# Optimization experiments

Hardware: AMD Instinct MI355X
Metric: run time of the kernel (lower is better)

Reference implementation:

```python
import jax, jax.numpy as jnp
import numpy as np

N_EMBD = 768
NUM_EXPERTS = 64
EXPERT_WIDTH = 256            # all experts uniform width (expert_sizes=[(64,256)])
TOTAL_WIDTH = NUM_EXPERTS * EXPERT_WIDTH  # 16384
TOP_K = 8


def setup_inputs() -> dict:
    key = jax.random.key(0)
    k1, k2, k3, k4 = jax.random.split(key, 4)
    B, S = 1, 2048
    x = jax.random.normal(k1, (B, S, N_EMBD), dtype=jnp.float32)
    # router: nn.Linear(n_embd, num_experts, bias=False) -> weight [E, n_embd]
    router_w = jax.random.normal(k2, (NUM_EXPERTS, N_EMBD), dtype=jnp.float32) * 0.02
    # trunc_normal(std=0.02) approximated by clipped normal
    w1 = jnp.clip(jax.random.normal(k3, (N_EMBD, TOTAL_WIDTH), dtype=jnp.float32) * 0.02, -0.06, 0.06)
    w2 = jnp.clip(jax.random.normal(k4, (TOTAL_WIDTH, N_EMBD), dtype=jnp.float32) * 0.02, -0.06, 0.06)
    return {"x": x, "router_w": router_w, "w1": w1, "w2": w2}


def reference(x, router_w, w1, w2):
    B, S, D = x.shape
    T = B * S
    x_flat = x.reshape(T, D)

    # Router: sigmoid gating + top-k
    router_logits = x_flat @ router_w.T                      # [T, E]
    router_probs = jax.nn.sigmoid(router_logits.astype(jnp.float32))
    top_k_weights, selected_experts = jax.lax.top_k(router_probs, TOP_K)  # [T, K]
    top_k_weights = top_k_weights / (top_k_weights.sum(axis=-1, keepdims=True) + 1e-20)
    top_k_weights = top_k_weights.astype(x.dtype)

    # Per-token expert combine weights [T, E]: 0 for unselected experts.
    tok_idx = jnp.arange(T)[:, None]
    w_tok = jnp.zeros((T, NUM_EXPERTS), dtype=x.dtype).at[tok_idx, selected_experts].set(top_k_weights)

    # Expert MLP (relu^2 activation), dense-masked equivalent of
    # padded_gather -> grouped GEMM -> padded_scatter.
    h = jnp.square(jax.nn.relu(x_flat @ w1))                 # [T, E*W]
    h = (h.reshape(T, NUM_EXPERTS, EXPERT_WIDTH) * w_tok[:, :, None]).reshape(T, TOTAL_WIDTH)
    output = (h @ w2).reshape(B, S, D)

    # Aux losses
    router_z_loss = jnp.mean(jnp.square(jax.nn.logsumexp(router_logits, axis=-1)))
    tokens_per_expert = jnp.zeros((NUM_EXPERTS,), dtype=jnp.float32).at[selected_experts.reshape(-1)].add(1.0)
    f_i = (tokens_per_expert / tokens_per_expert.sum()).astype(x.dtype)
    p_i = router_probs.mean(axis=0)
    # all expert widths equal -> num_experts * (f_i . p_i)
    load_balance_loss = NUM_EXPERTS * (f_i.astype(jnp.float32) @ p_i)
    # expert_widths_normalized == ones -> mean over tokens of sum of probs
    compute_loss = router_probs.sum(axis=-1).mean()

    return output, router_z_loss, load_balance_loss, compute_loss, f_i
```

## Files before the change

### kernel.cpp

```cpp
#include <hip/hip_runtime.h>
#include <hip/hip_bf16.h>

#define T_TOKENS 2048
#define D_EMBD 768
#define N_EXP 64
#define EW 256
#define TOPK 8
#define TW (N_EXP*EW)
#define PAD_SLOTS 20480
#define SCHED_MAX 2560
#define OUT_BASE (2048*768)

typedef __attribute__((ext_vector_type(8))) short bf16x8;
typedef __attribute__((ext_vector_type(4))) float f32x4;

typedef __attribute__((address_space(1))) void GAS;
typedef __attribute__((address_space(3))) void LAS;
#define GLOAD16(g, l) __builtin_amdgcn_global_load_lds((GAS*)(g), (LAS*)(l), 16, 0, 0)

__global__ void k_init(int* counts, int* cursor, float* psum, float* scal,
                       float* wgt_slot, int* tok_slot, int* sched_e) {
  int i = blockIdx.x*256 + threadIdx.x;
  if (i < N_EXP) { counts[i] = 0; cursor[i] = 0; psum[i] = 0.f; }
  if (i < 2) scal[i] = 0.f;
  if (i < PAD_SLOTS) { wgt_slot[i] = 0.f; tok_slot[i] = 0; }
  if (i < SCHED_MAX) sched_e[i] = -1;
}

__global__ void k_cvt_x(const float* __restrict__ x, __hip_bfloat16* __restrict__ xb) {
  int i = blockIdx.x*256 + threadIdx.x;
  float4 v = reinterpret_cast<const float4*>(x)[i];
  union { __hip_bfloat16 b; unsigned short u; } c0, c1, c2, c3;
  c0.b = __float2bfloat16(v.x); c1.b = __float2bfloat16(v.y);
  c2.b = __float2bfloat16(v.z); c3.b = __float2bfloat16(v.w);
  ushort4 o; o.x = c0.u; o.y = c1.u; o.z = c2.u; o.w = c3.u;
  reinterpret_cast<ushort4*>(xb)[i] = o;
}

__global__ __launch_bounds__(256) void k_transpose_cvt(
    const float* __restrict__ s1, __hip_bfloat16* __restrict__ d1,
    const float* __restrict__ s2, __hip_bfloat16* __restrict__ d2) {
  __shared__ float t[64][65];
  const float* src; __hip_bfloat16* dst; int R, C, bx, by;
  if (blockIdx.z == 0) { src = s1; dst = d1; R = 768; C = 16384;
                         bx = blockIdx.x*64; by = blockIdx.y*64; }
  else                 { src = s2; dst = d2; R = 16384; C = 768;
                         bx = blockIdx.y*64; by = blockIdx.x*64; }
  int tid = threadIdx.x;
  int lr = tid >> 4, lc4 = tid & 15;
  #pragma unroll
  for (int i = 0; i < 4; i++) {
    int r = lr + i*16;
    float4 v = *reinterpret_cast<const float4*>(&src[(size_t)(by+r)*C + bx + lc4*4]);
    t[r][lc4*4+0] = v.x; t[r][lc4*4+1] = v.y; t[r][lc4*4+2] = v.z; t[r][lc4*4+3] = v.w;
  }
  __syncthreads();
  int a = tid & 7, b0 = tid >> 3;
  int r0 = a*8;
  #pragma unroll
  for (int pass = 0; pass < 2; pass++) {
    int c = b0 + pass*32;
    unsigned int w[8];
    #pragma unroll
    for (int j = 0; j < 8; j++) {
      union { __hip_bfloat16 b; unsigned short u; } cv;
      cv.b = __float2bfloat16(t[r0+j][c]);
      w[j] = cv.u;
    }
    uint4 o;
    o.x = w[0] | (w[1] << 16);
    o.y = w[2] | (w[3] << 16);
    o.z = w[4] | (w[5] << 16);
    o.w = w[6] | (w[7] << 16);
    *reinterpret_cast<uint4*>(&dst[(size_t)(bx+c)*R + by + r0]) = o;
  }
}

__global__ __launch_bounds__(256) void k_logits(const float* __restrict__ x,
                                                const float* __restrict__ rw,
                                                float* __restrict__ lp) {
  __shared__ float rw_s[8][256];
  int tid = threadIdx.x;
  int tg = blockIdx.x, eg = blockIdx.y, kc = blockIdx.z;
  #pragma unroll
  for (int idx = 0; idx < 8; idx++)
    rw_s[idx][tid] = rw[(size_t)(eg*8 + idx)*D_EMBD + kc*256 + tid];
  __syncthreads();
  int tok = tg*256 + tid;
  const float4* x4 = reinterpret_cast<const float4*>(x + (size_t)tok*D_EMBD + kc*256);
  float acc[8];
  #pragma unroll
  for (int e = 0; e < 8; e++) acc[e] = 0.f;
  #pragma unroll 4
  for (int k4 = 0; k4 < 64; k4++) {
    float4 xv = x4[k4];
    #pragma unroll
    for (int e = 0; e < 8; e++)
      acc[e] += xv.x*rw_s[e][k4*4+0] + xv.y*rw_s[e][k4*4+1]
              + xv.z*rw_s[e][k4*4+2] + xv.w*rw_s[e][k4*4+3];
  }
  float* dst = lp + (size_t)kc*T_TOKENS*N_EXP + (size_t)tok*N_EXP + eg*8;
  float4 o0 = {acc[0], acc[1], acc[2], acc[3]};
  float4 o1 = {acc[4], acc[5], acc[6], acc[7]};
  reinterpret_cast<float4*>(dst)[0] = o0;
  reinterpret_cast<float4*>(dst)[1] = o1;
}

__global__ __launch_bounds__(256) void k_router2(const float* __restrict__ lp,
                          int* __restrict__ sel_e, float* __restrict__ sel_w,
                          int* __restrict__ counts, float* __restrict__ psum,
                          float* __restrict__ scal) {
  __shared__ float psum_s[4][64];
  __shared__ int cnt_s[4][64];
  int tid = threadIdx.x, wv = tid >> 6, lane = tid & 63;
  float pacc = 0.f, zacc = 0.f;
  int cacc = 0;
  int tbase = blockIdx.x*8 + wv*2;
  #pragma unroll
  for (int it = 0; it < 2; it++) {
    int t = tbase + it;
    float logit = lp[(size_t)t*N_EXP + lane]
                + lp[(size_t)T_TOKENS*N_EXP + (size_t)t*N_EXP + lane]
                + lp[2*(size_t)T_TOKENS*N_EXP + (size_t)t*N_EXP + lane];
    float prob = 1.f/(1.f + expf(-logit));
    pacc += prob;
    float mx = logit;
    for (int s = 32; s; s >>= 1) mx = fmaxf(mx, __shfl_xor(mx, s, 64));
    float sse = expf(logit - mx);
    for (int s = 32; s; s >>= 1) sse += __shfl_xor(sse, s, 64);
    float lse = mx + logf(sse);
    zacc += lse*lse;
    int rank = 0;
    #pragma unroll
    for (int j = 0; j < 64; j++) {
      float pj = __shfl(prob, j, 64);
      rank += (pj > prob || (pj == prob && j < lane)) ? 1 : 0;
    }
    bool sel = rank < TOPK;
    float sp = sel ? prob : 0.f;
    for (int s = 32; s; s >>= 1) sp += __shfl_xor(sp, s, 64);
    if (sel) {
      sel_e[t*TOPK + rank] = lane;
      sel_w[t*TOPK + rank] = prob / (sp + 1e-20f);
      cacc++;
    }
  }
  psum_s[wv][lane] = pacc;
  cnt_s[wv][lane] = cacc;
  if (lane == 0) atomicAdd(&scal[0], zacc);
  __syncthreads();
  if (tid < 64) {
    float p = psum_s[0][tid] + psum_s[1][tid] + psum_s[2][tid] + psum_s[3][tid];
    int c = cnt_s[0][tid] + cnt_s[1][tid] + cnt_s[2][tid] + cnt_s[3][tid];
    atomicAdd(&psum[tid], p);
    atomicAdd(&counts[tid], c);
  }
}

__global__ void k_schedule(const int* __restrict__ counts, int* __restrict__ offsets,
                           int* __restrict__ sched_e, int* __restrict__ sched_r0) {
  int e = threadIdx.x;
  int c = counts[e];
  int tiles = (c + 63) >> 6;
  int padded = tiles << 6;
  int ip = padded;
  for (int s = 1; s < 64; s <<= 1) { int v = __shfl_up(ip, s, 64); if (e >= s) ip += v; }
  int rowoff = ip - padded;
  offsets[e] = rowoff;
  int it = tiles;
  for (int s = 8; s < 64; s <<= 1) { int v = __shfl_up(it, s, 64); if (e >= s) it += v; }
  int rank = it - tiles;
  int xcd = e & 7;
  for (int i = 0; i < tiles; i++) {
    int p = xcd + 8*(rank + i);
    sched_e[p] = e;
    sched_r0[p] = rowoff + i*64;
  }
}

__global__ void k_assign(const int* __restrict__ sel_e, const float* __restrict__ sel_w,
                         const int* __restrict__ offsets, int* __restrict__ cursor,
                         int* __restrict__ tok_slot, float* __restrict__ wgt_slot,
                         int* __restrict__ slot_tk) {
  int i = blockIdx.x*256 + threadIdx.x;
  int e = sel_e[i];
  int pos = atomicAdd(&cursor[e], 1);
  int slot = offsets[e] + pos;
  tok_slot[slot] = i >> 3;
  wgt_slot[slot] = sel_w[i];
  slot_tk[i] = slot;
}

template<int MODE>
__global__ __launch_bounds__(256) void k_moe_gemm(
    const __hip_bfloat16* __restrict__ Ab, const __hip_bfloat16* __restrict__ Bt,
    const int* __restrict__ sched_e, const int* __restrict__ sched_r0,
    const int* __restrict__ tok_slot, const float* __restrict__ wgt_slot,
    __hip_bfloat16* __restrict__ outp) {
  constexpr int NS = (MODE == 1) ? 12 : 4;
  __shared__ __hip_bfloat16 As[2][64*64];
  __shared__ __hip_bfloat16 Bs[2][128*64];
  int tid = threadIdx.x;
  int nch = blockIdx.y;
  int arl = tid >> 3, akc = tid & 7;
  int a_off = ((akc ^ (arl & 7)) << 3);
  int b_off = a_off;
  int wv = tid >> 6, lane = tid & 63;
  int wm = wv >> 1, wn = wv & 1;
  int l15 = lane & 15, l4 = lane >> 4;
  int b_str = (MODE == 1) ? D_EMBD : TW;

  for (int p = blockIdx.x; p < SCHED_MAX; p += gridDim.x) {
    int e = sched_e[p];
    if (e < 0) continue;
    int r0 = sched_r0[p];

    size_t a_base0, a_base1;
    if (MODE == 1) {
      a_base0 = (size_t)tok_slot[r0 + arl] * D_EMBD;
      a_base1 = (size_t)tok_slot[r0 + arl + 32] * D_EMBD;
    } else {
      a_base0 = (size_t)(r0 + arl) * EW;
      a_base1 = (size_t)(r0 + arl + 32) * EW;
    }
    size_t b_base = (MODE == 1) ? (size_t)(e*EW + nch*128) * D_EMBD
                                : (size_t)(nch*128) * TW + (size_t)e*EW;

    f32x4 acc[2][4];
    f32x4 z = {0.f, 0.f, 0.f, 0.f};
    #pragma unroll
    for (int m = 0; m < 2; m++)
      #pragma unroll
      for (int n = 0; n < 4; n++) acc[m][n] = z;

    auto STAGE = [&](int bsel, int k0) {
      GLOAD16(Ab + a_base0 + k0 + a_off, &As[bsel][0] + tid*8);
      GLOAD16(Ab + a_base1 + k0 + a_off, &As[bsel][0] + (256 + tid)*8);
      #pragma unroll
      for (int i = 0; i < 4; i++) {
        int br = i*32 + arl;
        GLOAD16(Bt + b_base + (size_t)br*b_str + k0 + b_off, &Bs[bsel][0] + (i*256 + tid)*8);
      }
    };

    int cur = 0;
    STAGE(0, 0);
    asm volatile("s_waitcnt vmcnt(0)" ::: "memory");
    __syncthreads();
    for (int step = 0; step < NS; step++) {
      if (step + 1 < NS) STAGE(cur ^ 1, (step + 1)*64);
      const bf16x8* A8 = reinterpret_cast<const bf16x8*>(&As[cur][0]);
      const bf16x8* B8 = reinterpret_cast<const bf16x8*>(&Bs[cur][0]);
      bf16x8 af[2][2], bq[4][2];
      #pragma unroll
      for (int m = 0; m < 2; m++) {
        int ra = wm*32 + m*16 + l15;
        #pragma unroll
        for (int kk = 0; kk < 2; kk++)
          af[m][kk] = A8[ra*8 + ((kk*4 + l4) ^ (ra & 7))];
      }
      #pragma unroll
      for (int n = 0; n < 4; n++) {
        int rb = wn*64 + n*16 + l15;
        #pragma unroll
        for (int kk = 0; kk < 2; kk++)
          bq[n][kk] = B8[rb*8 + ((kk*4 + l4) ^ (rb & 7))];
      }
      #pragma unroll
      for (int kk = 0; kk < 2; kk++)
        #pragma unroll
        for (int m = 0; m < 2; m++)
          #pragma unroll
          for (int n = 0; n < 4; n++)
            acc[m][n] = __builtin_amdgcn_mfma_f32_16x16x32_bf16(af[m][kk], bq[n][kk], acc[m][n], 0, 0, 0);
      asm volatile("s_waitcnt vmcnt(0)" ::: "memory");
      __syncthreads();
      cur ^= 1;
    }

    if (MODE == 1) {
      #pragma unroll
      for (int m = 0; m < 2; m++)
        #pragma unroll
        for (int j = 0; j < 4; j++) {
          int r = r0 + wm*32 + m*16 + l4*4 + j;
          float wg = wgt_slot[r];
          #pragma unroll
          for (int n = 0; n < 4; n++) {
            int col = nch*128 + wn*64 + n*16 + l15;
            float v = fmaxf(acc[m][n][j], 0.f);
            outp[(size_t)r*EW + col] = __float2bfloat16(v*v*wg);
          }
        }
    } else {
      #pragma unroll
      for (int m = 0; m < 2; m++)
        #pragma unroll
        for (int j = 0; j < 4; j++) {
          int r = r0 + wm*32 + m*16 + l4*4 + j;
          #pragma unroll
          for (int n = 0; n < 4; n++) {
            int col = nch*128 + wn*64 + n*16 + l15;
            outp[(size_t)r*D_EMBD + col] = __float2bfloat16(acc[m][n][j]);
          }
        }
    }
  }
}

__global__ void k_combine(const __hip_bfloat16* __restrict__ y, const int* __restrict__ slot_tk,
                          float* __restrict__ out) {
  __shared__ int s[TOPK];
  int t = blockIdx.x, tid = threadIdx.x;
  if (tid < TOPK) s[tid] = slot_tk[t*TOPK + tid];
  __syncthreads();
  if (tid < 192) {
    int c = tid*4;
    float a0 = 0.f, a1 = 0.f, a2 = 0.f, a3 = 0.f;
    #pragma unroll
    for (int k = 0; k < TOPK; k++) {
      ushort4 v = *reinterpret_cast<const ushort4*>(&y[(size_t)s[k]*D_EMBD + c]);
      union { unsigned int u; float f; } f0, f1, f2, f3;
      f0.u = ((unsigned int)v.x) << 16;
      f1.u = ((unsigned int)v.y) << 16;
      f2.u = ((unsigned int)v.z) << 16;
      f3.u = ((unsigned int)v.w) << 16;
      a0 += f0.f; a1 += f1.f; a2 += f2.f; a3 += f3.f;
    }
    float4 o = {a0, a1, a2, a3};
    *reinterpret_cast<float4*>(&out[(size_t)t*D_EMBD + c]) = o;
  }
}

__global__ void k_finalize(const int* __restrict__ counts, const float* __restrict__ psum,
                           const float* __restrict__ scal, float* __restrict__ out) {
  __shared__ float part[N_EXP], ptot[N_EXP];
  int e = threadIdx.x;
  float f = (float)counts[e] / 16384.f;
  float p = psum[e] / 2048.f;
  part[e] = f * p;
  ptot[e] = p;
  out[OUT_BASE + 3 + e] = f;
  __syncthreads();
  if (e == 0) {
    float s = 0.f, q = 0.f;
    for (int i = 0; i < N_EXP; i++) { s += part[i]; q += ptot[i]; }
    out[OUT_BASE + 0] = scal[0] / 2048.f;
    out[OUT_BASE + 1] = 64.f * s;
    out[OUT_BASE + 2] = q;
  }
}

extern "C" void kernel_launch(void* const* d_in, const int* in_sizes, int n_in,
                              void* d_out, int out_size, void* d_ws, size_t ws_size,
                              hipStream_t stream) {
  const float* x  = (const float*)d_in[0];
  const float* rw = (const float*)d_in[1];
  const float* w1 = (const float*)d_in[2];
  const float* w2 = (const float*)d_in[3];
  float* out = (float*)d_out;
  char* ws = (char*)d_ws;

  size_t o = 0;
  auto alloc = [&](size_t b) { size_t r = o; o += (b + 255) & ~(size_t)255; return r; };
  __hip_bfloat16* xb    = (__hip_bfloat16*)(ws + alloc(2048UL*768*2));
  __hip_bfloat16* w1t   = (__hip_bfloat16*)(ws + alloc(16384UL*768*2));
  __hip_bfloat16* w2t   = (__hip_bfloat16*)(ws + alloc(768UL*16384*2));
  __hip_bfloat16* hprm  = (__hip_bfloat16*)(ws + alloc((size_t)PAD_SLOTS*256*2));
  __hip_bfloat16* yprm  = (__hip_bfloat16*)(ws + alloc((size_t)PAD_SLOTS*768*2));
  float* lp      = (float*)(ws + alloc(3UL*2048*64*4));
  int*   sel_e   = (int*)  (ws + alloc(16384UL*4));
  float* sel_w   = (float*)(ws + alloc(16384UL*4));
  int*   slot_tk = (int*)  (ws + alloc(16384UL*4));
  int*   tokslot = (int*)  (ws + alloc((size_t)PAD_SLOTS*4));
  float* wgtslot = (float*)(ws + alloc((size_t)PAD_SLOTS*4));
  int*   counts  = (int*)  (ws + alloc(256));
  int*   cursor  = (int*)  (ws + alloc(256));
  float* psum    = (float*)(ws + alloc(256));
  float* scal    = (float*)(ws + alloc(256));
  int*   offsets = (int*)  (ws + alloc(256));
  int*   sch_e   = (int*)  (ws + alloc(SCHED_MAX*4));
  int*   sch_r0  = (int*)  (ws + alloc(SCHED_MAX*4));

  k_init<<<80, 256, 0, stream>>>(counts, cursor, psum, scal, wgtslot, tokslot, sch_e);
  k_cvt_x<<<1536, 256, 0, stream>>>(x, xb);
  k_transpose_cvt<<<dim3(256, 12, 2), 256, 0, stream>>>(w1, w1t, w2, w2t);
  k_logits<<<dim3(8, 8, 3), 256, 0, stream>>>(x, rw, lp);
  k_router2<<<256, 256, 0, stream>>>(lp, sel_e, sel_w, counts, psum, scal);
  k_schedule<<<1, 64, 0, stream>>>(counts, offsets, sch_e, sch_r0);
  k_assign<<<64, 256, 0, stream>>>(sel_e, sel_w, offsets, cursor, tokslot, wgtslot, slot_tk);
  k_moe_gemm<1><<<dim3(512, 2), 256, 0, stream>>>(xb, w1t, sch_e, sch_r0, tokslot, wgtslot, hprm);
  k_moe_gemm<2><<<dim3(512, 6), 256, 0, stream>>>(hprm, w2t, sch_e, sch_r0, tokslot, wgtslot, yprm);
  k_combine<<<2048, 256, 0, stream>>>(yprm, slot_tk, out);
  k_finalize<<<1, 64, 0, stream>>>(counts, psum, scal, out);
}
```

Baseline: 143.4 us.

## Shrink MoE row tiles to 32, keep GEMM2 A-tile resident, batch transpose tiles

Expert row padding drops from 64 to 32 rows, which cuts wasted padded rows in both grouped GEMMs. The schedule array grows to match. GEMM2 now loads the full 32x256 A tile into LDS once and loops over three 128-column output chunks per block, instead of reloading A for each of six y-blocks. The weight transpose kernel handles four 64x64 tiles per block and prefetches the next tile's loads into registers while converting the current one. Smaller M tiles halve the MFMA work per B-tile load, so weight traffic per useful FLOP goes up.

Result: slower. 164.8 us (+14.9%).

```diff
diff --git a/kernel.cpp b/kernel.cpp
--- a/kernel.cpp
+++ b/kernel.cpp
@@ -8,7 +8,7 @@
 #define TOPK 8
 #define TW (N_EXP*EW)
 #define PAD_SLOTS 20480
-#define SCHED_MAX 2560
+#define SCHED_MAX 4608
 #define OUT_BASE (2048*768)
 
 typedef __attribute__((ext_vector_type(8))) short bf16x8;
@@ -41,38 +41,57 @@
     const float* __restrict__ s1, __hip_bfloat16* __restrict__ d1,
     const float* __restrict__ s2, __hip_bfloat16* __restrict__ d2) {
   __shared__ float t[64][65];
-  const float* src; __hip_bfloat16* dst; int R, C, bx, by;
+  const float* src; __hip_bfloat16* dst; int R, C;
+  int ro_base, co_base, ro_step, co_step;
   if (blockIdx.z == 0) { src = s1; dst = d1; R = 768; C = 16384;
-                         bx = blockIdx.x*64; by = blockIdx.y*64; }
+                         ro_base = blockIdx.y*64; co_base = blockIdx.x*256;
+                         ro_step = 0; co_step = 64; }
   else                 { src = s2; dst = d2; R = 16384; C = 768;
-                         bx = blockIdx.y*64; by = blockIdx.x*64; }
+                         ro_base = blockIdx.x*256; co_base = blockIdx.y*64;
+                         ro_step = 64; co_step = 0; }
   int tid = threadIdx.x;
   int lr = tid >> 4, lc4 = tid & 15;
+  int a = tid & 7, b0 = tid >> 3;
+
+  float4 v[4];
   #pragma unroll
-  for (int i = 0; i < 4; i++) {
-    int r = lr + i*16;
-    float4 v = *reinterpret_cast<const float4*>(&src[(size_t)(by+r)*C + bx + lc4*4]);
-    t[r][lc4*4+0] = v.x; t[r][lc4*4+1] = v.y; t[r][lc4*4+2] = v.z; t[r][lc4*4+3] = v.w;
-  }
-  __syncthreads();
-  int a = tid & 7, b0 = tid >> 3;
-  int r0 = a*8;
-  #pragma unroll
-  for (int pass = 0; pass < 2; pass++) {
-    int c = b0 + pass*32;
-    unsigned int w[8];
-    #pragma unroll
-    for (int j = 0; j < 8; j++) {
-      union { __hip_bfloat16 b; unsigned short u; } cv;
-      cv.b = __float2bfloat16(t[r0+j][c]);
-      w[j] = cv.u;
-    }
-    uint4 o;
-    o.x = w[0] | (w[1] << 16);
-    o.y = w[2] | (w[3] << 16);
-    o.z = w[4] | (w[5] << 16);
-    o.w = w[6] | (w[7] << 16);
-    *reinterpret_cast<uint4*>(&dst[(size_t)(bx+c)*R + by + r0]) = o;
+  for (int i = 0; i < 4; i++)
+    v[i] = *reinterpret_cast<const float4*>(&src[(size_t)(ro_base + lr + i*16)*C + co_base + lc4*4]);
+
+  for (int q = 0; q < 4; q++) {
+    int ro = ro_base + q*ro_step, co = co_base + q*co_step;
+    __syncthreads();
+    #pragma unroll
+    for (int i = 0; i < 4; i++) {
+      int r = lr + i*16;
+      t[r][lc4*4+0] = v[i].x; t[r][lc4*4+1] = v[i].y;
+      t[r][lc4*4+2] = v[i].z; t[r][lc4*4+3] = v[i].w;
+    }
+    __syncthreads();
+    if (q < 3) {
+      int ro2 = ro_base + (q+1)*ro_step, co2 = co_base + (q+1)*co_step;
+      #pragma unroll
+      for (int i = 0; i < 4; i++)
+        v[i] = *reinterpret_cast<const float4*>(&src[(size_t)(ro2 + lr + i*16)*C + co2 + lc4*4]);
+    }
+    int r0 = a*8;
+    #pragma unroll
+    for (int pass = 0; pass < 2; pass++) {
+      int c = b0 + pass*32;
+      unsigned int w[8];
+      #pragma unroll
+      for (int j = 0; j < 8; j++) {
+        union { __hip_bfloat16 b; unsigned short u; } cv;
+        cv.b = __float2bfloat16(t[r0+j][c]);
+        w[j] = cv.u;
+      }
+      uint4 o;
+      o.x = w[0] | (w[1] << 16);
+      o.y = w[2] | (w[3] << 16);
+      o.z = w[4] | (w[5] << 16);
+      o.w = w[6] | (w[7] << 16);
+      *reinterpret_cast<uint4*>(&dst[(size_t)(co + c)*R + ro + r0]) = o;
+    }
   }
 }
 
@@ -161,8 +180,8 @@
                            int* __restrict__ sched_e, int* __restrict__ sched_r0) {
   int e = threadIdx.x;
   int c = counts[e];
-  int tiles = (c + 63) >> 6;
-  int padded = tiles << 6;
+  int tiles = (c + 31) >> 5;
+  int padded = tiles << 5;
   int ip = padded;
   for (int s = 1; s < 64; s <<= 1) { int v = __shfl_up(ip, s, 64); if (e >= s) ip += v; }
   int rowoff = ip - padded;
@@ -174,7 +193,7 @@
   for (int i = 0; i < tiles; i++) {
     int p = xcd + 8*(rank + i);
     sched_e[p] = e;
-    sched_r0[p] = rowoff + i*64;
+    sched_r0[p] = rowoff + i*32;
   }
 }
 
@@ -191,55 +210,40 @@
   slot_tk[i] = slot;
 }
 
-template<int MODE>
-__global__ __launch_bounds__(256) void k_moe_gemm(
+__global__ __launch_bounds__(256) void k_gemm1(
     const __hip_bfloat16* __restrict__ Ab, const __hip_bfloat16* __restrict__ Bt,
     const int* __restrict__ sched_e, const int* __restrict__ sched_r0,
     const int* __restrict__ tok_slot, const float* __restrict__ wgt_slot,
     __hip_bfloat16* __restrict__ outp) {
-  constexpr int NS = (MODE == 1) ? 12 : 4;
-  __shared__ __hip_bfloat16 As[2][64*64];
+  __shared__ __hip_bfloat16 As[2][32*64];
   __shared__ __hip_bfloat16 Bs[2][128*64];
   int tid = threadIdx.x;
   int nch = blockIdx.y;
   int arl = tid >> 3, akc = tid & 7;
   int a_off = ((akc ^ (arl & 7)) << 3);
-  int b_off = a_off;
   int wv = tid >> 6, lane = tid & 63;
   int wm = wv >> 1, wn = wv & 1;
   int l15 = lane & 15, l4 = lane >> 4;
-  int b_str = (MODE == 1) ? D_EMBD : TW;
 
   for (int p = blockIdx.x; p < SCHED_MAX; p += gridDim.x) {
     int e = sched_e[p];
     if (e < 0) continue;
     int r0 = sched_r0[p];
 
-    size_t a_base0, a_base1;
-    if (MODE == 1) {
-      a_base0 = (size_t)tok_slot[r0 + arl] * D_EMBD;
-      a_base1 = (size_t)tok_slot[r0 + arl + 32] * D_EMBD;
-    } else {
-      a_base0 = (size_t)(r0 + arl) * EW;
-      a_base1 = (size_t)(r0 + arl + 32) * EW;
-    }
-    size_t b_base = (MODE == 1) ? (size_t)(e*EW + nch*128) * D_EMBD
-                                : (size_t)(nch*128) * TW + (size_t)e*EW;
-
-    f32x4 acc[2][4];
+    size_t a_base = (size_t)tok_slot[r0 + arl] * D_EMBD;
+    size_t b_base = (size_t)(e*EW + nch*128) * D_EMBD;
+
+    f32x4 acc[4];
     f32x4 z = {0.f, 0.f, 0.f, 0.f};
     #pragma unroll
-    for (int m = 0; m < 2; m++)
-      #pragma unroll
-      for (int n = 0; n < 4; n++) acc[m][n] = z;
+    for (int n = 0; n < 4; n++) acc[n] = z;
 
     auto STAGE = [&](int bsel, int k0) {
-      GLOAD16(Ab + a_base0 + k0 + a_off, &As[bsel][0] + tid*8);
-      GLOAD16(Ab + a_base1 + k0 + a_off, &As[bsel][0] + (256 + tid)*8);
+      GLOAD16(Ab + a_base + k0 + a_off, &As[bsel][0] + tid*8);
       #pragma unroll
       for (int i = 0; i < 4; i++) {
         int br = i*32 + arl;
-        GLOAD16(Bt + b_base + (size_t)br*b_str + k0 + b_off, &Bs[bsel][0] + (i*256 + tid)*8);
+        GLOAD16(Bt + b_base + (size_t)br*D_EMBD + k0 + a_off, &Bs[bsel][0] + (i*256 + tid)*8);
       }
     };
 
@@ -247,18 +251,15 @@
     STAGE(0, 0);
     asm volatile("s_waitcnt vmcnt(0)" ::: "memory");
     __syncthreads();
-    for (int step = 0; step < NS; step++) {
-      if (step + 1 < NS) STAGE(cur ^ 1, (step + 1)*64);
+    for (int step = 0; step < 12; step++) {
+      if (step + 1 < 12) STAGE(cur ^ 1, (step + 1)*64);
       const bf16x8* A8 = reinterpret_cast<const bf16x8*>(&As[cur][0]);
       const bf16x8* B8 = reinterpret_cast<const bf16x8*>(&Bs[cur][0]);
-      bf16x8 af[2][2], bq[4][2];
-      #pragma unroll
-      for (int m = 0; m < 2; m++) {
-        int ra = wm*32 + m*16 + l15;
-        #pragma unroll
-        for (int kk = 0; kk < 2; kk++)
-          af[m][kk] = A8[ra*8 + ((kk*4 + l4) ^ (ra & 7))];
-      }
+      bf16x8 af[2], bq[4][2];
+      int ra = wm*16 + l15;
+      #pragma unroll
+      for (int kk = 0; kk < 2; kk++)
+        af[kk] = A8[ra*8 + ((kk*4 + l4) ^ (ra & 7))];
       #pragma unroll
       for (int n = 0; n < 4; n++) {
         int rb = wn*64 + n*16 + l15;
@@ -269,41 +270,112 @@
       #pragma unroll
       for (int kk = 0; kk < 2; kk++)
         #pragma unroll
-        for (int m = 0; m < 2; m++)
-          #pragma unroll
-          for (int n = 0; n < 4; n++)
-            acc[m][n] = __builtin_amdgcn_mfma_f32_16x16x32_bf16(af[m][kk], bq[n][kk], acc[m][n], 0, 0, 0);
+        for (int n = 0; n < 4; n++)
+          acc[n] = __builtin_amdgcn_mfma_f32_16x16x32_bf16(af[kk], bq[n][kk], acc[n], 0, 0, 0);
       asm volatile("s_waitcnt vmcnt(0)" ::: "memory");
       __syncthreads();
       cur ^= 1;
     }
 
-    if (MODE == 1) {
-      #pragma unroll
-      for (int m = 0; m < 2; m++)
+    #pragma unroll
+    for (int j = 0; j < 4; j++) {
+      int r = r0 + wm*16 + l4*4 + j;
+      float wg = wgt_slot[r];
+      #pragma unroll
+      for (int n = 0; n < 4; n++) {
+        int col = nch*128 + wn*64 + n*16 + l15;
+        float v = fmaxf(acc[n][j], 0.f);
+        outp[(size_t)r*EW + col] = __float2bfloat16(v*v*wg);
+      }
+    }
+  }
+}
+
+__global__ __launch_bounds__(256) void k_gemm2(
+    const __hip_bfloat16* __restrict__ Ab, const __hip_bfloat16* __restrict__ Bt,
+    const int* __restrict__ sched_e, const int* __restrict__ sched_r0,
+    __hip_bfloat16* __restrict__ outp) {
+  __shared__ __hip_bfloat16 As[32*256];
+  __shared__ __hip_bfloat16 Bs[2][128*64];
+  int tid = threadIdx.x;
+  int ypair = blockIdx.y;
+  int arl = tid >> 3, akc = tid & 7;
+  int a_swz = (akc ^ (arl & 7));
+  int wv = tid >> 6, lane = tid & 63;
+  int wm = wv >> 1, wn = wv & 1;
+  int l15 = lane & 15, l4 = lane >> 4;
+
+  for (int p = blockIdx.x; p < SCHED_MAX; p += gridDim.x) {
+    int e = sched_e[p];
+    if (e < 0) continue;
+    int r0 = sched_r0[p];
+
+    size_t a_base = (size_t)(r0 + arl) * EW;
+    #pragma unroll
+    for (int i = 0; i < 4; i++)
+      GLOAD16(Ab + a_base + (i*8 + a_swz)*8, &As[0] + (i*256 + tid)*8);
+
+    auto STAGE_B = [&](int bsel, int nch, int k0) {
+      size_t b_base = (size_t)(nch*128) * TW + (size_t)e*EW;
+      #pragma unroll
+      for (int i = 0; i < 4; i++) {
+        int br = i*32 + arl;
+        GLOAD16(Bt + b_base + (size_t)br*TW + k0 + (a_swz << 3), &Bs[bsel][0] + (i*256 + tid)*8);
+      }
+    };
+
+    int cur = 0;
+    STAGE_B(0, ypair*3, 0);
+    asm volatile("s_waitcnt vmcnt(0)" ::: "memory");
+    __syncthreads();
+
+    f32x4 acc[4];
+    f32x4 z = {0.f, 0.f, 0.f, 0.f};
+    #pragma unroll
+    for (int n = 0; n < 4; n++) acc[n] = z;
+
+    for (int s = 0; s < 12; s++) {
+      int kstep = s & 3;
+      if (s + 1 < 12) {
+        int s1 = s + 1;
+        STAGE_B(cur ^ 1, ypair*3 + (s1 >> 2), (s1 & 3)*64);
+      }
+      const bf16x8* A8 = reinterpret_cast<const bf16x8*>(&As[0]);
+      const bf16x8* B8 = reinterpret_cast<const bf16x8*>(&Bs[cur][0]);
+      bf16x8 af[2], bq[4][2];
+      int ra = wm*16 + l15;
+      #pragma unroll
+      for (int kk = 0; kk < 2; kk++)
+        af[kk] = A8[kstep*256 + ra*8 + ((kk*4 + l4) ^ (ra & 7))];
+      #pragma unroll
+      for (int n = 0; n < 4; n++) {
+        int rb = wn*64 + n*16 + l15;
+        #pragma unroll
+        for (int kk = 0; kk < 2; kk++)
+          bq[n][kk] = B8[rb*8 + ((kk*4 + l4) ^ (rb & 7))];
+      }
+      #pragma unroll
+      for (int kk = 0; kk < 2; kk++)
+        #pragma unroll
+        for (int n = 0; n < 4; n++)
+          acc[n] = __builtin_amdgcn_mfma_f32_16x16x32_bf16(af[kk], bq[n][kk], acc[n], 0, 0, 0);
+      asm volatile("s_waitcnt vmcnt(0)" ::: "memory");
+      __syncthreads();
+      cur ^= 1;
+      if (kstep == 3) {
+        int nch = ypair*3 + (s >> 2);
         #pragma unroll
         for (int j = 0; j < 4; j++) {
-          int r = r0 + wm*32 + m*16 + l4*4 + j;
-          float wg = wgt_slot[r];
+          int r = r0 + wm*16 + l4*4 + j;
           #pragma unroll
           for (int n = 0; n < 4; n++) {
             int col = nch*128 + wn*64 + n*16 + l15;
-            float v = fmaxf(acc[m][n][j], 0.f);
-            outp[(size_t)r*EW + col] = __float2bfloat16(v*v*wg);
+            outp[(size_t)r*D_EMBD + col] = __float2bfloat16(acc[n][j]);
           }
         }
-    } else {
-      #pragma unroll
-      for (int m = 0; m < 2; m++)
-        #pragma unroll
-        for (int j = 0; j < 4; j++) {
-          int r = r0 + wm*32 + m*16 + l4*4 + j;
-          #pragma unroll
-          for (int n = 0; n < 4; n++) {
-            int col = nch*128 + wn*64 + n*16 + l15;
-            outp[(size_t)r*D_EMBD + col] = __float2bfloat16(acc[m][n][j]);
-          }
-        }
+        #pragma unroll
+        for (int n = 0; n < 4; n++) acc[n] = z;
+      }
     }
   }
 }
@@ -384,13 +456,13 @@
 
   k_init<<<80, 256, 0, stream>>>(counts, cursor, psum, scal, wgtslot, tokslot, sch_e);
   k_cvt_x<<<1536, 256, 0, stream>>>(x, xb);
-  k_transpose_cvt<<<dim3(256, 12, 2), 256, 0, stream>>>(w1, w1t, w2, w2t);
+  k_transpose_cvt<<<dim3(64, 12, 2), 256, 0, stream>>>(w1, w1t, w2, w2t);
   k_logits<<<dim3(8, 8, 3), 256, 0, stream>>>(x, rw, lp);
   k_router2<<<256, 256, 0, stream>>>(lp, sel_e, sel_w, counts, psum, scal);
   k_schedule<<<1, 64, 0, stream>>>(counts, offsets, sch_e, sch_r0);
   k_assign<<<64, 256, 0, stream>>>(sel_e, sel_w, offsets, cursor, tokslot, wgtslot, slot_tk);
-  k_moe_gemm<1><<<dim3(512, 2), 256, 0, stream>>>(xb, w1t, sch_e, sch_r0, tokslot, wgtslot, hprm);
-  k_moe_gemm<2><<<dim3(512, 6), 256, 0, stream>>>(hprm, w2t, sch_e, sch_r0, tokslot, wgtslot, yprm);
+  k_gemm1<<<dim3(512, 2), 256, 0, stream>>>(xb, w1t, sch_e, sch_r0, tokslot, wgtslot, hprm);
+  k_gemm2<<<dim3(512, 2), 256, 0, stream>>>(hprm, w2t, sch_e, sch_r0, yprm);
   k_combine<<<2048, 256, 0, stream>>>(yprm, slot_tk, out);
   k_finalize<<<1, 64, 0, stream>>>(counts, psum, scal, out);
 }
```

## Stream weight transposes per block to write full contiguous bf16 rows

Applied to the files above, without the earlier changes.

Replaces the 64x64-tile transpose-convert kernel with two templated kernels, one per weight. Each block walks many 64-row chunks, prefetching the next chunk into registers while converting the current one into a large XOR-swizzled LDS staging buffer. It then writes long contiguous destination rows (768 or 512 bf16 elements) instead of scattered 16-byte pieces. The aim is better write coalescing and fewer, larger blocks, at the cost of much more LDS per block (about 96KB or 64KB), which lowers occupancy, and two launches instead of one.

New measurement: 147.9 us. 3.2% more time.

```diff
diff --git a/kernel.cpp b/kernel.cpp
--- a/kernel.cpp
+++ b/kernel.cpp
@@ -37,42 +37,70 @@
   reinterpret_cast<ushort4*>(xb)[i] = o;
 }
 
-__global__ __launch_bounds__(256) void k_transpose_cvt(
-    const float* __restrict__ s1, __hip_bfloat16* __restrict__ d1,
-    const float* __restrict__ s2, __hip_bfloat16* __restrict__ d2) {
-  __shared__ float t[64][65];
-  const float* src; __hip_bfloat16* dst; int R, C, bx, by;
-  if (blockIdx.z == 0) { src = s1; dst = d1; R = 768; C = 16384;
-                         bx = blockIdx.x*64; by = blockIdx.y*64; }
-  else                 { src = s2; dst = d2; R = 16384; C = 768;
-                         bx = blockIdx.y*64; by = blockIdx.x*64; }
+template<int Z>
+__global__ __launch_bounds__(256) void k_transpose_stream(
+    const float* __restrict__ src, __hip_bfloat16* __restrict__ dst) {
+  constexpr int NCH   = (Z == 0) ? 12 : 8;
+  constexpr int ROWCH = NCH*8;
+  constexpr int C     = (Z == 0) ? 16384 : 768;
+  constexpr size_t DL = (Z == 0) ? 768 : 16384;
+  __shared__ float tb[64][65];
+  __shared__ __hip_bfloat16 ob[64*NCH*64];
+
+  int bid = blockIdx.x;
+  int n0, kbase;
+  if (Z == 0) { n0 = bid*64; kbase = 0; }
+  else        { n0 = (bid >> 5)*64; kbase = (bid & 31)*512; }
+
   int tid = threadIdx.x;
-  int lr = tid >> 4, lc4 = tid & 15;
+  int lr = tid >> 4, lc = (tid & 15)*4;
+  int n_l = tid & 63;
+  int k8b = (tid >> 6)*2;
+
+  float4 v[4];
   #pragma unroll
-  for (int i = 0; i < 4; i++) {
-    int r = lr + i*16;
-    float4 v = *reinterpret_cast<const float4*>(&src[(size_t)(by+r)*C + bx + lc4*4]);
-    t[r][lc4*4+0] = v.x; t[r][lc4*4+1] = v.y; t[r][lc4*4+2] = v.z; t[r][lc4*4+3] = v.w;
+  for (int i = 0; i < 4; i++)
+    v[i] = *reinterpret_cast<const float4*>(&src[(size_t)(kbase + lr + i*16)*C + n0 + lc]);
+
+  for (int c = 0; c < NCH; c++) {
+    __syncthreads();
+    #pragma unroll
+    for (int i = 0; i < 4; i++) {
+      int r = lr + i*16;
+      tb[r][lc+0] = v[i].x; tb[r][lc+1] = v[i].y;
+      tb[r][lc+2] = v[i].z; tb[r][lc+3] = v[i].w;
+    }
+    __syncthreads();
+    if (c + 1 < NCH) {
+      #pragma unroll
+      for (int i = 0; i < 4; i++)
+        v[i] = *reinterpret_cast<const float4*>(&src[(size_t)(kbase + (c+1)*64 + lr + i*16)*C + n0 + lc]);
+    }
+    #pragma unroll
+    for (int u = 0; u < 2; u++) {
+      int k8 = k8b + u;
+      unsigned int w[4];
+      #pragma unroll
+      for (int jj = 0; jj < 4; jj++) {
+        union { __hip_bfloat16 b; unsigned short us; } lo, hi;
+        lo.b = __float2bfloat16(tb[k8*8 + jj*2][n_l]);
+        hi.b = __float2bfloat16(tb[k8*8 + jj*2 + 1][n_l]);
+        w[jj] = (unsigned int)lo.us | ((unsigned int)hi.us << 16);
+      }
+      int chunk = (c*8 + k8) ^ (n_l & 7);
+      uint4 o = {w[0], w[1], w[2], w[3]};
+      *reinterpret_cast<uint4*>(reinterpret_cast<char*>(ob) + (size_t)n_l*(ROWCH*16) + chunk*16) = o;
+    }
   }
   __syncthreads();
-  int a = tid & 7, b0 = tid >> 3;
-  int r0 = a*8;
-  #pragma unroll
-  for (int pass = 0; pass < 2; pass++) {
-    int c = b0 + pass*32;
-    unsigned int w[8];
-    #pragma unroll
-    for (int j = 0; j < 8; j++) {
-      union { __hip_bfloat16 b; unsigned short u; } cv;
-      cv.b = __float2bfloat16(t[r0+j][c]);
-      w[j] = cv.u;
-    }
-    uint4 o;
-    o.x = w[0] | (w[1] << 16);
-    o.y = w[2] | (w[3] << 16);
-    o.z = w[4] | (w[5] << 16);
-    o.w = w[6] | (w[7] << 16);
-    *reinterpret_cast<uint4*>(&dst[(size_t)(bx+c)*R + by + r0]) = o;
+  constexpr int ROUNDS = NCH*2;
+  #pragma unroll 4
+  for (int r = 0; r < ROUNDS; r++) {
+    int f = r*256 + tid;
+    int n = f / ROWCH, kc = f % ROWCH;
+    uint4 o = *reinterpret_cast<const uint4*>(
+        reinterpret_cast<const char*>(ob) + (size_t)n*(ROWCH*16) + ((kc ^ (n & 7))*16));
+    *reinterpret_cast<uint4*>(&dst[(size_t)(n0 + n)*DL + kbase + kc*8]) = o;
   }
 }
 
@@ -384,7 +412,8 @@
 
   k_init<<<80, 256, 0, stream>>>(counts, cursor, psum, scal, wgtslot, tokslot, sch_e);
   k_cvt_x<<<1536, 256, 0, stream>>>(x, xb);
-  k_transpose_cvt<<<dim3(256, 12, 2), 256, 0, stream>>>(w1, w1t, w2, w2t);
+  k_transpose_stream<0><<<256, 256, 0, stream>>>(w1, w1t);
+  k_transpose_stream<1><<<384, 256, 0, stream>>>(w2, w2t);
   k_logits<<<dim3(8, 8, 3), 256, 0, stream>>>(x, rw, lp);
   k_router2<<<256, 256, 0, stream>>>(lp, sel_e, sel_w, counts, psum, scal);
   k_schedule<<<1, 64, 0, stream>>>(counts, offsets, sch_e, sch_r0);
```

## Fuse fp32-to-bf16 conversion and weight transpose into MoE GEMM tile loads

Applied to the files above, without the earlier changes.

Removes the separate x conversion and w1/w2 transpose-convert kernels. The grouped GEMMs now read fp32 activations and weights straight from global memory into registers, convert them to bf16, and write them into swizzled shared-memory tiles during the pipelined k-loop. This avoids a full pass over the weights each call (read fp32, write bf16) and two kernel launches. In exchange, the GEMMs read twice the bytes per weight element and replace async global-to-LDS loads with register staging, which adds register pressure and conversion work inside the main loop.

After: 143.8 us. Within noise of the previous version (+0.3%).

```diff
diff --git a/kernel.cpp b/kernel.cpp
--- a/kernel.cpp
+++ b/kernel.cpp
@@ -18,6 +18,13 @@
 typedef __attribute__((address_space(3))) void LAS;
 #define GLOAD16(g, l) __builtin_amdgcn_global_load_lds((GAS*)(g), (LAS*)(l), 16, 0, 0)
 
+__device__ inline unsigned short f2bu(float f) {
+  union { __hip_bfloat16 b; unsigned short u; } cv; cv.b = __float2bfloat16(f); return cv.u;
+}
+__device__ inline unsigned int pk2(float a, float b) {
+  return (unsigned int)f2bu(a) | ((unsigned int)f2bu(b) << 16);
+}
+
 __global__ void k_init(int* counts, int* cursor, float* psum, float* scal,
                        float* wgt_slot, int* tok_slot, int* sched_e) {
   int i = blockIdx.x*256 + threadIdx.x;
@@ -25,55 +32,6 @@
   if (i < 2) scal[i] = 0.f;
   if (i < PAD_SLOTS) { wgt_slot[i] = 0.f; tok_slot[i] = 0; }
   if (i < SCHED_MAX) sched_e[i] = -1;
-}
-
-__global__ void k_cvt_x(const float* __restrict__ x, __hip_bfloat16* __restrict__ xb) {
-  int i = blockIdx.x*256 + threadIdx.x;
-  float4 v = reinterpret_cast<const float4*>(x)[i];
-  union { __hip_bfloat16 b; unsigned short u; } c0, c1, c2, c3;
-  c0.b = __float2bfloat16(v.x); c1.b = __float2bfloat16(v.y);
-  c2.b = __float2bfloat16(v.z); c3.b = __float2bfloat16(v.w);
-  ushort4 o; o.x = c0.u; o.y = c1.u; o.z = c2.u; o.w = c3.u;
-  reinterpret_cast<ushort4*>(xb)[i] = o;
-}
-
-__global__ __launch_bounds__(256) void k_transpose_cvt(
-    const float* __restrict__ s1, __hip_bfloat16* __restrict__ d1,
-    const float* __restrict__ s2, __hip_bfloat16* __restrict__ d2) {
-  __shared__ float t[64][65];
-  const float* src; __hip_bfloat16* dst; int R, C, bx, by;
-  if (blockIdx.z == 0) { src = s1; dst = d1; R = 768; C = 16384;
-                         bx = blockIdx.x*64; by = blockIdx.y*64; }
-  else                 { src = s2; dst = d2; R = 16384; C = 768;
-                         bx = blockIdx.y*64; by = blockIdx.x*64; }
-  int tid = threadIdx.x;
-  int lr = tid >> 4, lc4 = tid & 15;
-  #pragma unroll
-  for (int i = 0; i < 4; i++) {
-    int r = lr + i*16;
-    float4 v = *reinterpret_cast<const float4*>(&src[(size_t)(by+r)*C + bx + lc4*4]);
-    t[r][lc4*4+0] = v.x; t[r][lc4*4+1] = v.y; t[r][lc4*4+2] = v.z; t[r][lc4*4+3] = v.w;
-  }
-  __syncthreads();
-  int a = tid & 7, b0 = tid >> 3;
-  int r0 = a*8;
-  #pragma unroll
-  for (int pass = 0; pass < 2; pass++) {
-    int c = b0 + pass*32;
-    unsigned int w[8];
-    #pragma unroll
-    for (int j = 0; j < 8; j++) {
-      union { __hip_bfloat16 b; unsigned short u; } cv;
-      cv.b = __float2bfloat16(t[r0+j][c]);
-      w[j] = cv.u;
-    }
-    uint4 o;
-    o.x = w[0] | (w[1] << 16);
-    o.y = w[2] | (w[3] << 16);
-    o.z = w[4] | (w[5] << 16);
-    o.w = w[6] | (w[7] << 16);
-    *reinterpret_cast<uint4*>(&dst[(size_t)(bx+c)*R + by + r0]) = o;
-  }
 }
 
 __global__ __launch_bounds__(256) void k_logits(const float* __restrict__ x,
@@ -193,38 +151,88 @@
 
 template<int MODE>
 __global__ __launch_bounds__(256) void k_moe_gemm(
-    const __hip_bfloat16* __restrict__ Ab, const __hip_bfloat16* __restrict__ Bt,
+    const void* __restrict__ Asrc, const float* __restrict__ Bsrc,
     const int* __restrict__ sched_e, const int* __restrict__ sched_r0,
     const int* __restrict__ tok_slot, const float* __restrict__ wgt_slot,
     __hip_bfloat16* __restrict__ outp) {
-  constexpr int NS = (MODE == 1) ? 12 : 4;
+  constexpr int NS   = (MODE == 1) ? 12 : 4;
+  constexpr int BSTR = (MODE == 1) ? TW : D_EMBD;
   __shared__ __hip_bfloat16 As[2][64*64];
   __shared__ __hip_bfloat16 Bs[2][128*64];
   int tid = threadIdx.x;
   int nch = blockIdx.y;
+  int n4 = tid & 31, kpb = tid >> 5;
+  int mrow = tid >> 4, k4f = tid & 15;
   int arl = tid >> 3, akc = tid & 7;
   int a_off = ((akc ^ (arl & 7)) << 3);
-  int b_off = a_off;
   int wv = tid >> 6, lane = tid & 63;
   int wm = wv >> 1, wn = wv & 1;
   int l15 = lane & 15, l4 = lane >> 4;
-  int b_str = (MODE == 1) ? D_EMBD : TW;
 
   for (int p = blockIdx.x; p < SCHED_MAX; p += gridDim.x) {
     int e = sched_e[p];
     if (e < 0) continue;
     int r0 = sched_r0[p];
 
-    size_t a_base0, a_base1;
+    int browb = (MODE == 1) ? 0 : e*EW;
+    int bcolb = (MODE == 1) ? (e*EW + nch*128) : nch*128;
+
+    int tks[4];
+    size_t a_base0 = 0, a_base1 = 0;
     if (MODE == 1) {
-      a_base0 = (size_t)tok_slot[r0 + arl] * D_EMBD;
-      a_base1 = (size_t)tok_slot[r0 + arl + 32] * D_EMBD;
+      #pragma unroll
+      for (int i = 0; i < 4; i++) tks[i] = tok_slot[r0 + i*16 + mrow];
     } else {
       a_base0 = (size_t)(r0 + arl) * EW;
       a_base1 = (size_t)(r0 + arl + 32) * EW;
     }
-    size_t b_base = (MODE == 1) ? (size_t)(e*EW + nch*128) * D_EMBD
-                                : (size_t)(nch*128) * TW + (size_t)e*EW;
+
+    float bv0[4][4], bv1[4][4], av[4][4];
+
+    auto B_LOAD = [&](int k0) {
+      #pragma unroll
+      for (int j = 0; j < 4; j++) {
+        const float* rp = Bsrc + (size_t)(browb + k0 + 2*(kpb + 8*j))*BSTR + bcolb + n4*4;
+        *reinterpret_cast<float4*>(&bv0[j][0]) = *reinterpret_cast<const float4*>(rp);
+        *reinterpret_cast<float4*>(&bv1[j][0]) = *reinterpret_cast<const float4*>(rp + BSTR);
+      }
+    };
+    auto B_WRITE = [&](int bsel) {
+      char* bs = (char*)&Bs[bsel][0];
+      #pragma unroll
+      for (int j = 0; j < 4; j++) {
+        int kp = kpb + 8*j;
+        #pragma unroll
+        for (int c = 0; c < 4; c++) {
+          int n = n4*4 + c;
+          int ch = (kp >> 2) ^ ((n & 7) ^ ((n >> 3) & 7));
+          *reinterpret_cast<unsigned int*>(bs + n*128 + ch*16 + (kp & 3)*4)
+              = pk2(bv0[j][c], bv1[j][c]);
+        }
+      }
+    };
+    auto A_LOAD1 = [&](int k0) {
+      const float* xf = (const float*)Asrc;
+      #pragma unroll
+      for (int i = 0; i < 4; i++)
+        *reinterpret_cast<float4*>(&av[i][0]) =
+            *reinterpret_cast<const float4*>(xf + (size_t)tks[i]*D_EMBD + k0 + k4f*4);
+    };
+    auto A_WRITE1 = [&](int bsel) {
+      char* as_ = (char*)&As[bsel][0];
+      #pragma unroll
+      for (int i = 0; i < 4; i++) {
+        int m = i*16 + mrow;
+        int ch = (k4f >> 1) ^ (m & 7);
+        uint2 val = { pk2(av[i][0], av[i][1]), pk2(av[i][2], av[i][3]) };
+        *reinterpret_cast<uint2*>(as_ + m*128 + ch*16 + (k4f & 1)*8) = val;
+      }
+    };
+    auto A_GLOAD2 = [&](int bsel, int k0) {
+      const __hip_bfloat16* hb = (const __hip_bfloat16*)Asrc;
+      GLOAD16(hb + a_base0 + k0 + a_off, &As[bsel][0] + tid*8);
+      GLOAD16(hb + a_base1 + k0 + a_off, &As[bsel][0] + (256 + tid)*8);
+    };
 
     f32x4 acc[2][4];
     f32x4 z = {0.f, 0.f, 0.f, 0.f};
@@ -233,38 +241,38 @@
       #pragma unroll
       for (int n = 0; n < 4; n++) acc[m][n] = z;
 
-    auto STAGE = [&](int bsel, int k0) {
-      GLOAD16(Ab + a_base0 + k0 + a_off, &As[bsel][0] + tid*8);
-      GLOAD16(Ab + a_base1 + k0 + a_off, &As[bsel][0] + (256 + tid)*8);
-      #pragma unroll
-      for (int i = 0; i < 4; i++) {
-        int br = i*32 + arl;
-        GLOAD16(Bt + b_base + (size_t)br*b_str + k0 + b_off, &Bs[bsel][0] + (i*256 + tid)*8);
-      }
-    };
+    if (MODE == 1) { A_LOAD1(0); B_LOAD(0); A_WRITE1(0); B_WRITE(0); }
+    else           { A_GLOAD2(0, 0); B_LOAD(0); B_WRITE(0);
+                     asm volatile("s_waitcnt vmcnt(0)" ::: "memory"); }
+    __syncthreads();
 
     int cur = 0;
-    STAGE(0, 0);
-    asm volatile("s_waitcnt vmcnt(0)" ::: "memory");
-    __syncthreads();
     for (int step = 0; step < NS; step++) {
-      if (step + 1 < NS) STAGE(cur ^ 1, (step + 1)*64);
-      const bf16x8* A8 = reinterpret_cast<const bf16x8*>(&As[cur][0]);
-      const bf16x8* B8 = reinterpret_cast<const bf16x8*>(&Bs[cur][0]);
+      bool more = (step + 1 < NS);
+      int k1 = (step + 1)*64;
+      if (more) {
+        if (MODE == 1) { A_LOAD1(k1); B_LOAD(k1); }
+        else           { A_GLOAD2(cur ^ 1, k1); B_LOAD(k1); }
+      }
+      const char* asC = (const char*)&As[cur][0];
+      const char* bsC = (const char*)&Bs[cur][0];
       bf16x8 af[2][2], bq[4][2];
       #pragma unroll
       for (int m = 0; m < 2; m++) {
         int ra = wm*32 + m*16 + l15;
         #pragma unroll
         for (int kk = 0; kk < 2; kk++)
-          af[m][kk] = A8[ra*8 + ((kk*4 + l4) ^ (ra & 7))];
+          af[m][kk] = *reinterpret_cast<const bf16x8*>(
+              asC + ra*128 + (((kk*4 + l4) ^ (ra & 7)) << 4));
       }
       #pragma unroll
       for (int n = 0; n < 4; n++) {
         int rb = wn*64 + n*16 + l15;
+        int Sb = (rb & 7) ^ ((rb >> 3) & 7);
         #pragma unroll
         for (int kk = 0; kk < 2; kk++)
-          bq[n][kk] = B8[rb*8 + ((kk*4 + l4) ^ (rb & 7))];
+          bq[n][kk] = *reinterpret_cast<const bf16x8*>(
+              bsC + rb*128 + (((kk*4 + l4) ^ Sb) << 4));
       }
       #pragma unroll
       for (int kk = 0; kk < 2; kk++)
@@ -273,7 +281,11 @@
           #pragma unroll
           for (int n = 0; n < 4; n++)
             acc[m][n] = __builtin_amdgcn_mfma_f32_16x16x32_bf16(af[m][kk], bq[n][kk], acc[m][n], 0, 0, 0);
-      asm volatile("s_waitcnt vmcnt(0)" ::: "memory");
+      if (more) {
+        if (MODE == 1) { A_WRITE1(cur ^ 1); B_WRITE(cur ^ 1); }
+        else           { B_WRITE(cur ^ 1);
+                         asm volatile("s_waitcnt vmcnt(0)" ::: "memory"); }
+      }
       __syncthreads();
       cur ^= 1;
     }
@@ -363,9 +375,6 @@
 
   size_t o = 0;
   auto alloc = [&](size_t b) { size_t r = o; o += (b + 255) & ~(size_t)255; return r; };
-  __hip_bfloat16* xb    = (__hip_bfloat16*)(ws + alloc(2048UL*768*2));
-  __hip_bfloat16* w1t   = (__hip_bfloat16*)(ws + alloc(16384UL*768*2));
-  __hip_bfloat16* w2t   = (__hip_bfloat16*)(ws + alloc(768UL*16384*2));
   __hip_bfloat16* hprm  = (__hip_bfloat16*)(ws + alloc((size_t)PAD_SLOTS*256*2));
   __hip_bfloat16* yprm  = (__hip_bfloat16*)(ws + alloc((size_t)PAD_SLOTS*768*2));
   float* lp      = (float*)(ws + alloc(3UL*2048*64*4));
@@ -383,14 +392,12 @@
   int*   sch_r0  = (int*)  (ws + alloc(SCHED_MAX*4));
 
   k_init<<<80, 256, 0, stream>>>(counts, cursor, psum, scal, wgtslot, tokslot, sch_e);
-  k_cvt_x<<<1536, 256, 0, stream>>>(x, xb);
-  k_transpose_cvt<<<dim3(256, 12, 2), 256, 0, stream>>>(w1, w1t, w2, w2t);
   k_logits<<<dim3(8, 8, 3), 256, 0, stream>>>(x, rw, lp);
   k_router2<<<256, 256, 0, stream>>>(lp, sel_e, sel_w, counts, psum, scal);
   k_schedule<<<1, 64, 0, stream>>>(counts, offsets, sch_e, sch_r0);
   k_assign<<<64, 256, 0, stream>>>(sel_e, sel_w, offsets, cursor, tokslot, wgtslot, slot_tk);
-  k_moe_gemm<1><<<dim3(512, 2), 256, 0, stream>>>(xb, w1t, sch_e, sch_r0, tokslot, wgtslot, hprm);
-  k_moe_gemm<2><<<dim3(512, 6), 256, 0, stream>>>(hprm, w2t, sch_e, sch_r0, tokslot, wgtslot, yprm);
+  k_moe_gemm<1><<<dim3(512, 2), 256, 0, stream>>>((const void*)x, w1, sch_e, sch_r0, tokslot, wgtslot, hprm);
+  k_moe_gemm<2><<<dim3(512, 6), 256, 0, stream>>>((const void*)hprm, w2, sch_e, sch_r0, tokslot, wgtslot, yprm);
   k_combine<<<2048, 256, 0, stream>>>(yprm, slot_tk, out);
   k_finalize<<<1, 64, 0, stream>>>(counts, psum, scal, out);
 }
```
